# Optimization experiments

Measured on AMD Instinct MI355X. Metric: run time of the kernel, lower is better.

## Reference

```python
import jax, jax.numpy as jnp
import numpy as np
from jax.ops import segment_sum

EPS = 1e-5
N, E = 100000, 1600000
CIN, H, COUT, ED = 32, 64, 16, 16


def _lin(k, fan_in, fan_out):
    return jax.random.normal(k, (fan_in, fan_out), jnp.float32) / np.sqrt(fan_in)


def setup_inputs() -> dict:
    key = jax.random.key(0)
    ks = jax.random.split(key, 24)
    inp = {
        "x": jax.random.normal(ks[0], (N, CIN), jnp.float32),
        "edge_index": jax.random.randint(ks[1], (2, E), 0, N, jnp.int32),
        "edge_attr": jax.random.normal(ks[2], (E, ED), jnp.float32),
    }
    # layer 1 (SAGEConvWithEdgeAttr: in=CIN -> H)
    inp.update(
        l1_Wl=_lin(ks[3], CIN, H), l1_bl=jnp.zeros((H,), jnp.float32),
        l1_Wr=_lin(ks[4], CIN, H),
        l1_We=_lin(ks[5], ED, H), l1_be=jnp.zeros((H,), jnp.float32),
        l1_Wg=_lin(ks[6], 2 * H, H), l1_bg=jnp.zeros((H,), jnp.float32),
        l1_bng=jnp.ones((H,), jnp.float32), l1_bnb=jnp.zeros((H,), jnp.float32),
    )
    # layer 2 (H -> H)
    inp.update(
        l2_Wl=_lin(ks[7], H, H), l2_bl=jnp.zeros((H,), jnp.float32),
        l2_Wr=_lin(ks[8], H, H),
        l2_We=_lin(ks[9], ED, H), l2_be=jnp.zeros((H,), jnp.float32),
        l2_Wg=_lin(ks[10], 2 * H, H), l2_bg=jnp.zeros((H,), jnp.float32),
        l2_bng=jnp.ones((H,), jnp.float32), l2_bnb=jnp.zeros((H,), jnp.float32),
    )
    # GraphNorms (weight=1, bias=0, mean_scale=1 at init; randomize slightly via ones)
    inp.update(
        gn1_g=jnp.ones((H,), jnp.float32), gn1_b=jnp.zeros((H,), jnp.float32), gn1_a=jnp.ones((H,), jnp.float32),
        gn2_g=jnp.ones((H,), jnp.float32), gn2_b=jnp.zeros((H,), jnp.float32), gn2_a=jnp.ones((H,), jnp.float32),
        lin_W=_lin(ks[11], H, COUT), lin_b=jnp.zeros((COUT,), jnp.float32),
    )
    return inp


def _sage_edge_layer(x, row, col, ea, Wl, bl, Wr, We, be, Wg, bg, bng, bnb):
    n = x.shape[0]
    ea_t = ea @ We + be                                        # [E', H]
    deg = segment_sum(jnp.ones_like(col, dtype=x.dtype), col, num_segments=n)
    agg = segment_sum(x[row], col, num_segments=n) / jnp.maximum(deg, 1.0)[:, None]
    out = agg @ Wl + bl + x @ Wr                               # SAGEConv (mean)
    gate = jax.nn.sigmoid(jnp.concatenate([out[col], ea_t], -1) @ Wg + bg)
    out = out + segment_sum(gate * ea_t, col, num_segments=n)  # edge contributions
    mu = out.mean(0)
    var = ((out - mu) ** 2).mean(0)                            # BatchNorm1d (batch stats)
    out = bng * (out - mu) * jax.lax.rsqrt(var + EPS) + bnb
    return jax.nn.relu(2.0 * out)                              # Identity residual + out, relu


def _graph_norm(x, g, b, a):
    mu = x.mean(0)
    xc = x - a * mu
    var = (xc ** 2).mean(0)
    return g * xc * jax.lax.rsqrt(var + EPS) + b


def reference(x, edge_index, edge_attr,
              l1_Wl, l1_bl, l1_Wr, l1_We, l1_be, l1_Wg, l1_bg, l1_bng, l1_bnb,
              l2_Wl, l2_bl, l2_Wr, l2_We, l2_be, l2_Wg, l2_bg, l2_bng, l2_bnb,
              gn1_g, gn1_b, gn1_a, gn2_g, gn2_b, gn2_a, lin_W, lin_b):
    n = x.shape[0]
    loop = jnp.arange(n, dtype=edge_index.dtype)
    row = jnp.concatenate([edge_index[0], loop])               # add_self_loops
    col = jnp.concatenate([edge_index[1], loop])
    ea = jnp.concatenate([edge_attr, jnp.ones((n, edge_attr.shape[1]), edge_attr.dtype)], 0)
    h = _sage_edge_layer(x, row, col, ea, l1_Wl, l1_bl, l1_Wr, l1_We, l1_be, l1_Wg, l1_bg, l1_bng, l1_bnb)
    h = jax.nn.relu(h)
    h = jax.nn.relu(_graph_norm(h, gn1_g, gn1_b, gn1_a))
    h = _sage_edge_layer(h, row, col, ea, l2_Wl, l2_bl, l2_Wr, l2_We, l2_be, l2_Wg, l2_bg, l2_bng, l2_bnb)
    h = jax.nn.relu(h)
    h = jax.nn.relu(_graph_norm(h, gn2_g, gn2_b, gn2_a))
    return h @ lin_W + lin_b
```

## Files before the change

### kernel.cpp

```cpp
#include <hip/hip_runtime.h>
#include <hip/hip_fp16.h>
#include <math.h>
#include <stdint.h>

#define H 64
#define ED 16
#define CO 16
#define WGRID 2048
#define NWAVES (WGRID * 4)
#define CPART 2048
static constexpr float EPSV = 1e-5f;
static constexpr float LOG2E = 1.44269504f;

typedef _Float16 h2v __attribute__((ext_vector_type(2)));

__device__ __forceinline__ float sigm2(float z) {
    return __builtin_amdgcn_rcpf(1.0f + __builtin_amdgcn_exp2f(-z));
}

__device__ __forceinline__ h2v as_h2(int x) { union { int i; h2v h; } u; u.i = x; return u.h; }

__device__ __forceinline__ int pack2(float a, float b) {
    __half2 h = __floats2half2_rn(a, b);
    return *reinterpret_cast<int*>(&h);
}

__global__ void k_prep(const float* __restrict__ We1, const float* __restrict__ be1, const float* __restrict__ Wg1,
                       const float* __restrict__ We2, const float* __restrict__ be2, const float* __restrict__ Wg2,
                       float* __restrict__ ws) {
    int j = threadIdx.x;
    for (int l = 0; l < 2; ++l) {
        const float* We = l ? We2 : We1;
        const float* be = l ? be2 : be1;
        const float* Wg = l ? Wg2 : Wg1;
        int* wth = (int*)(ws + (l ? 1024 : 0));
        int* wgh = (int*)(ws + (l ? 1536 : 512));
        float* ets = ws + 2048 + l * 192;
        float* vs  = ws + 2112 + l * 192;
        float* dv  = ws + 2176 + l * 192;
        float wt[ED], wg[ED];
        float et = be[j];
        for (int k = 0; k < ED; ++k) { wt[k] = We[k * H + j]; et += wt[k]; }
        ets[j] = et;
        float d = 0.f;
        for (int m = 0; m < H; ++m) d += be[m] * Wg[(H + m) * H + j];
        float vsum = d;
        for (int k = 0; k < ED; ++k) {
            float acc = 0.f;
            for (int m = 0; m < H; ++m) acc += We[k * H + m] * Wg[(H + m) * H + j];
            wg[k] = acc;
            vsum += acc;
        }
        dv[j] = d * LOG2E;
        vs[j] = vsum * LOG2E;
        for (int q = 0; q < 8; ++q) {
            wth[j * 8 + q] = pack2(wt[2 * q], wt[2 * q + 1]);
            wgh[j * 8 + q] = pack2(wg[2 * q] * LOG2E, wg[2 * q + 1] * LOG2E);
        }
    }
    for (int s = 0; s < 8; ++s) ws[2432 + s * 64 + j] = 0.f;
}

__global__ void k_xh(const float* __restrict__ x, __half* __restrict__ xh, int total4) {
    int i = blockIdx.x * blockDim.x + threadIdx.x;
    if (i >= total4) return;
    float4 v = *reinterpret_cast<const float4*>(x + (size_t)i * 4);
    __half2 h0 = __floats2half2_rn(v.x, v.y), h1 = __floats2half2_rn(v.z, v.w);
    uint2 o;
    o.x = *reinterpret_cast<unsigned*>(&h0);
    o.y = *reinterpret_cast<unsigned*>(&h1);
    *reinterpret_cast<uint2*>(xh + (size_t)i * 4) = o;
}

__global__ void k_count(const int* __restrict__ cols, int* __restrict__ cnt, int E) {
    int e = blockIdx.x * blockDim.x + threadIdx.x;
    if (e < E) atomicAdd(&cnt[cols[e]], 1);
}

__global__ __launch_bounds__(1024) void k_scan1(const int* __restrict__ cnt, int* __restrict__ bs, int N) {
    __shared__ int ls[1024];
    int t = threadIdx.x;
    int i = blockIdx.x * 1024 + t;
    ls[t] = (i < N) ? cnt[i] : 0;
    __syncthreads();
    for (int off = 512; off > 0; off >>= 1) {
        if (t < off) ls[t] += ls[t + off];
        __syncthreads();
    }
    if (t == 0) bs[blockIdx.x] = ls[0];
}

__global__ __launch_bounds__(1024) void k_scan2(int* __restrict__ bs, int SB) {
    __shared__ int ls[1024];
    int t = threadIdx.x;
    int v = (t < SB) ? bs[t] : 0;
    ls[t] = v;
    __syncthreads();
    for (int off = 1; off < 1024; off <<= 1) {
        int x = (t >= off) ? ls[t - off] : 0;
        __syncthreads();
        ls[t] += x;
        __syncthreads();
    }
    if (t < SB) bs[t] = ls[t] - v;
}

__global__ __launch_bounds__(1024) void k_scan3(const int* __restrict__ cnt, const int* __restrict__ bs,
                                                int* __restrict__ rowptr, int N, int E) {
    __shared__ int ls[1024];
    int t = threadIdx.x;
    int i = blockIdx.x * 1024 + t;
    int v = (i < N) ? cnt[i] : 0;
    ls[t] = v;
    __syncthreads();
    for (int off = 1; off < 1024; off <<= 1) {
        int x = (t >= off) ? ls[t - off] : 0;
        __syncthreads();
        ls[t] += x;
        __syncthreads();
    }
    if (i < N) rowptr[i] = bs[blockIdx.x] + ls[t] - v;
    if (i == 0) rowptr[N] = E;
}

__global__ void k_ranges(const int* __restrict__ rowptr, int* __restrict__ ranges, int N, int E, int nw) {
    int w = blockIdx.x * blockDim.x + threadIdx.x;
    if (w > nw) return;
    if (w == nw) { ranges[nw] = N; return; }
    int t0 = (int)((long)E * w / nw);
    int lo = 0, hi = N;
    while (lo < hi) { int mid = (lo + hi) >> 1; if (rowptr[mid] < t0) lo = mid + 1; else hi = mid; }
    ranges[w] = lo;
}

__global__ __launch_bounds__(256) void k_part(const int* __restrict__ rows, const int* __restrict__ cols,
                                              int2* __restrict__ tmp, int* __restrict__ offtab,
                                              int E, int NB, int SH) {
    __shared__ int hist[1025];
    __shared__ int pscan[256];
    __shared__ int2 stage[CPART];
    int tid = threadIdx.x;
    int base = blockIdx.x * CPART;
    int cnt = min(CPART, E - base);
    for (int i = tid; i <= NB; i += 256) hist[i] = 0;
    __syncthreads();
    int myc[8], myr[8];
#pragma unroll
    for (int q = 0; q < 8; ++q) {
        int li = q * 256 + tid;
        if (li < cnt) {
            int e = base + li;
            myc[q] = cols[e];
            myr[q] = rows[e];
            atomicAdd(&hist[myc[q] >> SH], 1);
        } else myc[q] = -1;
    }
    __syncthreads();
    int h[4], s = 0;
    int b0 = tid * 4;
#pragma unroll
    for (int k = 0; k < 4; ++k) { h[k] = (b0 + k < NB) ? hist[b0 + k] : 0; s += h[k]; }
    pscan[tid] = s;
    __syncthreads();
    for (int off = 1; off < 256; off <<= 1) {
        int v = (tid >= off) ? pscan[tid - off] : 0;
        __syncthreads();
        pscan[tid] += v;
        __syncthreads();
    }
    int excl = pscan[tid] - s;
    __syncthreads();
    int run = excl;
#pragma unroll
    for (int k = 0; k < 4; ++k) {
        if (b0 + k < NB) hist[b0 + k] = run;
        run += h[k];
    }
    __syncthreads();
    int* ot = offtab + (size_t)blockIdx.x * (NB + 1);
    for (int i = tid; i < NB; i += 256) ot[i] = hist[i];
    if (tid == 0) ot[NB] = cnt;
    __syncthreads();
    int mask = (1 << SH) - 1;
#pragma unroll
    for (int q = 0; q < 8; ++q) {
        if (myc[q] >= 0) {
            int b = myc[q] >> SH;
            int p = atomicAdd(&hist[b], 1);
            int e = base + q * 256 + tid;
            stage[p] = make_int2(myr[q], (e << SH) | (myc[q] & mask));
        }
    }
    __syncthreads();
    int2* dst = tmp + base;
    for (int i = tid; i < cnt; i += 256) dst[i] = stage[i];
}

__global__ __launch_bounds__(256) void k_build(const int* __restrict__ rowptr, const int2* __restrict__ tmp,
                                               const int* __restrict__ offtab, const float* __restrict__ ea,
                                               int* __restrict__ erow, __half* __restrict__ eap,
                                               int N, int NB, int SH, int PB) {
    __shared__ int lcur[1024];
    int tid = threadIdx.x;
    int b = blockIdx.x;
    int NPB = 1 << SH;
    int nodelo = b << SH;
    for (int j = tid; j < NPB; j += 256) {
        int n = nodelo + j;
        lcur[j] = (n < N) ? rowptr[n] : 0;
    }
    __syncthreads();
    int mask = NPB - 1;
    for (int i = tid; i < PB; i += 256) {
        const int* ot = offtab + (size_t)i * (NB + 1);
        int j0 = ot[b], j1 = ot[b + 1];
        for (int j = j0; j < j1; ++j) {
            int2 v = tmp[(size_t)i * CPART + j];
            int e = (int)(((unsigned)v.y) >> SH);
            int cl = v.y & mask;
            int p = atomicAdd(&lcur[cl], 1);
            erow[p] = v.x;
            const float4* src = reinterpret_cast<const float4*>(ea + (size_t)e * ED);
            float4 v0 = src[0], v1 = src[1], v2 = src[2], v3 = src[3];
            int hh[8];
            hh[0] = pack2(v0.x, v0.y); hh[1] = pack2(v0.z, v0.w);
            hh[2] = pack2(v1.x, v1.y); hh[3] = pack2(v1.z, v1.w);
            hh[4] = pack2(v2.x, v2.y); hh[5] = pack2(v2.z, v2.w);
            hh[6] = pack2(v3.x, v3.y); hh[7] = pack2(v3.z, v3.w);
            const int4* o = reinterpret_cast<const int4*>(hh);
            int4* d = reinterpret_cast<int4*>(eap + (size_t)p * ED);
            d[0] = o[0]; d[1] = o[1];
        }
    }
}

template <int CIN, bool GN>
__global__ __launch_bounds__(256) void k_gather(const __half* __restrict__ x, const int* __restrict__ rowptr,
                         const int* __restrict__ ranges,
                         const int* __restrict__ erow, float* __restrict__ agg,
                         const float* __restrict__ s1, const float* __restrict__ s2,
                         const float* __restrict__ gng, const float* __restrict__ gnb,
                         const float* __restrict__ gna, float Ninv, int N) {
    int lane = threadIdx.x & 63;
    int w = (blockIdx.x * blockDim.x + threadIdx.x) >> 6;
    float A = 1.f, B = 0.f;
    if (GN) {
        float mu = s1[lane] * Ninv, m2 = s2[lane] * Ninv, a = gna[lane];
        float var = m2 - 2.f * a * mu * mu + a * a * mu * mu;
        A = gng[lane] * rsqrtf(var + EPSV);
        B = gnb[lane] - A * a * mu;
    }
    int n0 = ranges[w], n1 = ranges[w + 1];
    for (int n = n0; n < n1; ++n) {
        int s = rowptr[n], te = rowptr[n + 1];
        if (CIN == 64) {
            float raw = __half2float(x[(size_t)n * 64 + lane]);
            float acc = GN ? fmaxf(fmaf(A, raw, B), 0.f) : raw;
            int i = s;
            for (; i + 7 < te; i += 8) {
                int r0 = erow[i],     r1 = erow[i + 1], r2 = erow[i + 2], r3 = erow[i + 3];
                int r4 = erow[i + 4], r5 = erow[i + 5], r6 = erow[i + 6], r7 = erow[i + 7];
                float x0 = __half2float(x[(size_t)r0 * 64 + lane]);
                float x1 = __half2float(x[(size_t)r1 * 64 + lane]);
                float x2 = __half2float(x[(size_t)r2 * 64 + lane]);
                float x3 = __half2float(x[(size_t)r3 * 64 + lane]);
                float x4 = __half2float(x[(size_t)r4 * 64 + lane]);
                float x5 = __half2float(x[(size_t)r5 * 64 + lane]);
                float x6 = __half2float(x[(size_t)r6 * 64 + lane]);
                float x7 = __half2float(x[(size_t)r7 * 64 + lane]);
                if (GN) {
                    x0 = fmaxf(fmaf(A, x0, B), 0.f); x1 = fmaxf(fmaf(A, x1, B), 0.f);
                    x2 = fmaxf(fmaf(A, x2, B), 0.f); x3 = fmaxf(fmaf(A, x3, B), 0.f);
                    x4 = fmaxf(fmaf(A, x4, B), 0.f); x5 = fmaxf(fmaf(A, x5, B), 0.f);
                    x6 = fmaxf(fmaf(A, x6, B), 0.f); x7 = fmaxf(fmaf(A, x7, B), 0.f);
                }
                acc += ((x0 + x1) + (x2 + x3)) + ((x4 + x5) + (x6 + x7));
            }
            for (; i < te; ++i) {
                float xv = __half2float(x[(size_t)erow[i] * 64 + lane]);
                if (GN) xv = fmaxf(fmaf(A, xv, B), 0.f);
                acc += xv;
            }
            agg[(size_t)n * H + lane] = acc;
        } else {
            int c = lane & 31, half = lane >> 5;
            float acc = half ? 0.f : __half2float(x[(size_t)n * 32 + c]);
            int i = s + half;
            for (; i + 6 < te; i += 8) {
                int r0 = erow[i], r1 = erow[i + 2], r2 = erow[i + 4], r3 = erow[i + 6];
                float x0 = __half2float(x[(size_t)r0 * 32 + c]);
                float x1 = __half2float(x[(size_t)r1 * 32 + c]);
                float x2 = __half2float(x[(size_t)r2 * 32 + c]);
                float x3 = __half2float(x[(size_t)r3 * 32 + c]);
                acc += (x0 + x1) + (x2 + x3);
            }
            for (; i < te; i += 2) acc += __half2float(x[(size_t)erow[i] * 32 + c]);
            acc += __shfl_xor(acc, 32);
            if (half == 0) agg[(size_t)n * H + c] = acc;
        }
    }
}

#define MT4A(mq, aval) \
    acc[mq][0] = fmaf(aval, w1.x, acc[mq][0]); acc[mq][1] = fmaf(aval, w1.y, acc[mq][1]); \
    acc[mq][2] = fmaf(aval, w1.z, acc[mq][2]); acc[mq][3] = fmaf(aval, w1.w, acc[mq][3]);
#define MT4X(mq, aval) \
    acc[mq][0] = fmaf(aval, w2.x, acc[mq][0]); acc[mq][1] = fmaf(aval, w2.y, acc[mq][1]); \
    acc[mq][2] = fmaf(aval, w2.z, acc[mq][2]); acc[mq][3] = fmaf(aval, w2.w, acc[mq][3]);

template <int K, bool GN>
__global__ __launch_bounds__(256) void k_gemmfu(
        const float* __restrict__ A,
        const __half* __restrict__ A2, int lda2,
        const float* __restrict__ W1, const float* __restrict__ W2,
        const float* __restrict__ bias,
        const float* __restrict__ Wg, const float* __restrict__ bg,
        const float* __restrict__ s1, const float* __restrict__ s2,
        const float* __restrict__ gng, const float* __restrict__ gnb,
        const float* __restrict__ gna, float Ninv,
        const int* __restrict__ rowptr,
        __half* __restrict__ pre, __half* __restrict__ uout, int N) {
    __shared__ float WA[64 * 64];
    __shared__ float WB[K * 64];
    __shared__ float big[64][68];
    __shared__ float As[64], Bs[64], invd[64];
    int tid = threadIdx.x;
    for (int idx = tid; idx < K * 64; idx += 256) { WA[idx] = W1[idx]; WB[idx] = W2[idx]; }
    int nb = blockIdx.x * 64;
    if (tid < 64) {
        if (GN) {
            float mu = s1[tid] * Ninv, m2 = s2[tid] * Ninv, a = gna[tid];
            float var = m2 - 2.f * a * mu * mu + a * a * mu * mu;
            float Av = gng[tid] * rsqrtf(var + EPSV);
            As[tid] = Av; Bs[tid] = gnb[tid] - Av * a * mu;
        }
        int n = nb + tid;
        invd[tid] = (n < N) ? 1.f / (float)(rowptr[n + 1] - rowptr[n] + 1) : 0.f;
    }
    __syncthreads();
    int tm = tid >> 4, tn = tid & 15;
    int m0 = tm * 4, j0 = tn * 4;
    float acc[4][4];
#pragma unroll
    for (int jq = 0; jq < 4; ++jq) {
        float b = bias[j0 + jq];
#pragma unroll
        for (int mq = 0; mq < 4; ++mq) acc[mq][jq] = b;
    }
    int sn = tid >> 2, kq4 = (tid & 3) * 4;
    int sg = nb + sn;
    for (int k0 = 0; k0 < K; k0 += 16) {
        if (k0) __syncthreads();
        if (sg < N) {
            float4 av = *reinterpret_cast<const float4*>(A + (size_t)sg * 64 + k0 + kq4);
            float sc = invd[sn];
            av.x *= sc; av.y *= sc; av.z *= sc; av.w *= sc;
            big[kq4 + 0][sn] = av.x; big[kq4 + 1][sn] = av.y;
            big[kq4 + 2][sn] = av.z; big[kq4 + 3][sn] = av.w;
            uint2 hv = *reinterpret_cast<const uint2*>(A2 + (size_t)sg * lda2 + k0 + kq4);
            __half2 h01 = *reinterpret_cast<__half2*>(&hv.x);
            __half2 h23 = *reinterpret_cast<__half2*>(&hv.y);
            float2 f01 = __half22float2(h01), f23 = __half22float2(h23);
            float xv0 = f01.x, xv1 = f01.y, xv2 = f23.x, xv3 = f23.y;
            if (GN) {
                xv0 = fmaxf(fmaf(As[k0 + kq4 + 0], xv0, Bs[k0 + kq4 + 0]), 0.f);
                xv1 = fmaxf(fmaf(As[k0 + kq4 + 1], xv1, Bs[k0 + kq4 + 1]), 0.f);
                xv2 = fmaxf(fmaf(As[k0 + kq4 + 2], xv2, Bs[k0 + kq4 + 2]), 0.f);
                xv3 = fmaxf(fmaf(As[k0 + kq4 + 3], xv3, Bs[k0 + kq4 + 3]), 0.f);
            }
            big[16 + kq4 + 0][sn] = xv0; big[16 + kq4 + 1][sn] = xv1;
            big[16 + kq4 + 2][sn] = xv2; big[16 + kq4 + 3][sn] = xv3;
        } else {
#pragma unroll
            for (int q = 0; q < 4; ++q) { big[kq4 + q][sn] = 0.f; big[16 + kq4 + q][sn] = 0.f; }
        }
        __syncthreads();
#pragma unroll
        for (int k = 0; k < 16; ++k) {
            float4 am = *reinterpret_cast<const float4*>(&big[k][m0]);
            float4 w1 = *reinterpret_cast<const float4*>(&WA[(k0 + k) * 64 + j0]);
            MT4A(0, am.x) MT4A(1, am.y) MT4A(2, am.z) MT4A(3, am.w)
            float4 xm = *reinterpret_cast<const float4*>(&big[16 + k][m0]);
            float4 w2 = *reinterpret_cast<const float4*>(&WB[(k0 + k) * 64 + j0]);
            MT4X(0, xm.x) MT4X(1, xm.y) MT4X(2, xm.z) MT4X(3, xm.w)
        }
    }
    __syncthreads();
#pragma unroll
    for (int mq = 0; mq < 4; ++mq) {
        int n = nb + m0 + mq;
        if (n < N) {
            uint2 o;
            o.x = pack2(acc[mq][0], acc[mq][1]);
            o.y = pack2(acc[mq][2], acc[mq][3]);
            *reinterpret_cast<uint2*>(pre + (size_t)n * 64 + j0) = o;
        }
#pragma unroll
        for (int jq = 0; jq < 4; ++jq) big[j0 + jq][m0 + mq] = acc[mq][jq];
    }
    for (int idx = tid; idx < 4096; idx += 256) WA[idx] = Wg[idx] * LOG2E;
    __syncthreads();
    float acc2[4][4];
#pragma unroll
    for (int jq = 0; jq < 4; ++jq) {
        float b = bg[j0 + jq] * LOG2E;
#pragma unroll
        for (int mq = 0; mq < 4; ++mq) acc2[mq][jq] = b;
    }
#pragma unroll 8
    for (int k = 0; k < 64; ++k) {
        float4 pm = *reinterpret_cast<const float4*>(&big[k][m0]);
        float4 w1 = *reinterpret_cast<const float4*>(&WA[k * 64 + j0]);
        acc2[0][0] = fmaf(pm.x, w1.x, acc2[0][0]); acc2[0][1] = fmaf(pm.x, w1.y, acc2[0][1]);
        acc2[0][2] = fmaf(pm.x, w1.z, acc2[0][2]); acc2[0][3] = fmaf(pm.x, w1.w, acc2[0][3]);
        acc2[1][0] = fmaf(pm.y, w1.x, acc2[1][0]); acc2[1][1] = fmaf(pm.y, w1.y, acc2[1][1]);
        acc2[1][2] = fmaf(pm.y, w1.z, acc2[1][2]); acc2[1][3] = fmaf(pm.y, w1.w, acc2[1][3]);
        acc2[2][0] = fmaf(pm.z, w1.x, acc2[2][0]); acc2[2][1] = fmaf(pm.z, w1.y, acc2[2][1]);
        acc2[2][2] = fmaf(pm.z, w1.z, acc2[2][2]); acc2[2][3] = fmaf(pm.z, w1.w, acc2[2][3]);
        acc2[3][0] = fmaf(pm.w, w1.x, acc2[3][0]); acc2[3][1] = fmaf(pm.w, w1.y, acc2[3][1]);
        acc2[3][2] = fmaf(pm.w, w1.z, acc2[3][2]); acc2[3][3] = fmaf(pm.w, w1.w, acc2[3][3]);
    }
#pragma unroll
    for (int mq = 0; mq < 4; ++mq) {
        int n = nb + m0 + mq;
        if (n < N) {
            uint2 o;
            o.x = pack2(acc2[mq][0], acc2[mq][1]);
            o.y = pack2(acc2[mq][2], acc2[mq][3]);
            *reinterpret_cast<uint2*>(uout + (size_t)n * 64 + j0) = o;
        }
    }
}

__device__ __forceinline__ float edge_term(const int4& a, const int4& b,
                                           const h2v* wt, const h2v* wg,
                                           float be_l, float dv_l, float u_l) {
    int ua[8] = {a.x, a.y, a.z, a.w, b.x, b.y, b.z, b.w};
    float et = be_l, v = dv_l;
#pragma unroll
    for (int q = 0; q < 8; ++q) {
        h2v e = as_h2(ua[q]);
        et = __builtin_amdgcn_fdot2(e, wt[q], et, false);
        v  = __builtin_amdgcn_fdot2(e, wg[q], v, false);
    }
    return sigm2(u_l + v) * et;
}

__global__ __launch_bounds__(256) void k_gate(
        const int* __restrict__ rowptr, const int* __restrict__ ranges,
        const __half* __restrict__ eap,
        const int* __restrict__ wth, const int* __restrict__ wgh,
        const float* __restrict__ be, const float* __restrict__ dv,
        const float* __restrict__ ets, const float* __restrict__ vs,
        const __half* __restrict__ u, __half* __restrict__ pre,
        float* __restrict__ s1, float* __restrict__ s2, int N) {
    __shared__ __align__(16) int4 estage[4][128];
    __shared__ float ls[2][4][H];
    int lane = threadIdx.x & 63;
    int wv = threadIdx.x >> 6;
    int w = (blockIdx.x << 2) | wv;
    h2v wt[8], wg[8];
#pragma unroll
    for (int q = 0; q < 8; ++q) { wt[q] = as_h2(wth[lane * 8 + q]); wg[q] = as_h2(wgh[lane * 8 + q]); }
    float be_l = be[lane], dv_l = dv[lane], ets_l = ets[lane], vs_l = vs[lane];
    int n0 = ranges[w], n1 = ranges[w + 1];
    float s = 0.f, ss = 0.f;
    if (n0 < n1) {
        int4* dst = &estage[wv][0];
        const int4* gsrc = reinterpret_cast<const int4*>(eap);
        int e0 = rowptr[n0], e1 = rowptr[n1];
        int n = n0;
        int nend = rowptr[n0 + 1];
        size_t idx = (size_t)n * H + lane;
        float u_l = __half2float(u[idx]);
        float pv = __half2float(pre[idx]);
        float acc = sigm2(u_l + vs_l) * ets_l;
        {
            int bytes = min(64, e1 - e0) * 32;
            int4 p0, p1;
            if (lane * 16 < bytes) p0 = gsrc[(size_t)e0 * 2 + lane];
            if (1024 + lane * 16 < bytes) p1 = gsrc[(size_t)e0 * 2 + 64 + lane];
            if (lane * 16 < bytes) dst[lane] = p0;
            if (1024 + lane * 16 < bytes) dst[64 + lane] = p1;
        }
        for (int c = e0; c < e1; c += 64) {
            int cnt = min(64, e1 - c);
            int nbytes = (c + 64 < e1) ? min(64, e1 - c - 64) * 32 : 0;
            int4 p0, p1;
            if (lane * 16 < nbytes) p0 = gsrc[(size_t)(c + 64) * 2 + lane];
            if (1024 + lane * 16 < nbytes) p1 = gsrc[(size_t)(c + 64) * 2 + 64 + lane];
            for (int k = 0; k < cnt; ++k) {
                while (c + k == nend) {
                    float tval = pv + acc;
                    pre[idx] = __float2half(tval);
                    s += tval; ss += tval * tval;
                    ++n;
                    idx = (size_t)n * H + lane;
                    u_l = __half2float(u[idx]);
                    pv = __half2float(pre[idx]);
                    acc = sigm2(u_l + vs_l) * ets_l;
                    nend = rowptr[n + 1];
                }
                acc += edge_term(dst[k * 2], dst[k * 2 + 1], wt, wg, be_l, dv_l, u_l);
            }
            if (lane * 16 < nbytes) dst[lane] = p0;
            if (1024 + lane * 16 < nbytes) dst[64 + lane] = p1;
        }
        for (;;) {
            float tval = pv + acc;
            pre[idx] = __float2half(tval);
            s += tval; ss += tval * tval;
            ++n;
            if (n >= n1) break;
            idx = (size_t)n * H + lane;
            u_l = __half2float(u[idx]);
            pv = __half2float(pre[idx]);
            acc = sigm2(u_l + vs_l) * ets_l;
        }
    }
    ls[0][wv][lane] = s; ls[1][wv][lane] = ss;
    __syncthreads();
    if (threadIdx.x < H) {
        float a = ls[0][0][lane] + ls[0][1][lane] + ls[0][2][lane] + ls[0][3][lane];
        float b = ls[1][0][lane] + ls[1][1][lane] + ls[1][2][lane] + ls[1][3][lane];
        atomicAdd(&s1[lane], a);
        atomicAdd(&s2[lane], b);
    }
}

__global__ void k_apply(const __half* __restrict__ in, __half* __restrict__ outb,
                        const float* __restrict__ bng, const float* __restrict__ bnb,
                        const float* __restrict__ s1b, const float* __restrict__ s2b,
                        float* __restrict__ s1g, float* __restrict__ s2g, float Ninv, int N) {
    int j = threadIdx.x, ty = threadIdx.y;
    __shared__ float As[H], Bs[H];
    if (ty == 0) {
        float mu = s1b[j] * Ninv, var = s2b[j] * Ninv - mu * mu;
        float r = rsqrtf(var + EPSV);
        float A = 2.f * bng[j] * r;
        As[j] = A; Bs[j] = 2.f * (bnb[j] - bng[j] * r * mu);
    }
    __syncthreads();
    float A = As[j], B = Bs[j];
    float s = 0.f, ss = 0.f;
    for (int n = blockIdx.x * 4 + ty; n < N; n += gridDim.x * 4) {
        size_t idx = (size_t)n * H + j;
        float v = fmaxf(fmaf(A, __half2float(in[idx]), B), 0.f);
        outb[idx] = __float2half(v);
        s += v; ss += v * v;
    }
    __shared__ float ls[2][4][H];
    ls[0][ty][j] = s; ls[1][ty][j] = ss;
    __syncthreads();
    if (ty == 0) {
        float a = ls[0][0][j] + ls[0][1][j] + ls[0][2][j] + ls[0][3][j];
        float b = ls[1][0][j] + ls[1][1][j] + ls[1][2][j] + ls[1][3][j];
        atomicAdd(&s1g[j], a);
        atomicAdd(&s2g[j], b);
    }
}

__global__ __launch_bounds__(256) void k_final(const __half* __restrict__ hraw, const float* __restrict__ W,
                        const float* __restrict__ bias,
                        const float* __restrict__ s1, const float* __restrict__ s2,
                        const float* __restrict__ gng, const float* __restrict__ gnb,
                        const float* __restrict__ gna, float Ninv,
                        float* __restrict__ outp, int N) {
    __shared__ float As[H], Bs[H];
    if (threadIdx.x < H) {
        int j = threadIdx.x;
        float mu = s1[j] * Ninv, m2 = s2[j] * Ninv, a = gna[j];
        float var = m2 - 2.f * a * mu * mu + a * a * mu * mu;
        float A = gng[j] * rsqrtf(var + EPSV);
        As[j] = A; Bs[j] = gnb[j] - A * a * mu;
    }
    __syncthreads();
    int n = blockIdx.x * blockDim.x + threadIdx.x;
    if (n >= N) return;
    float o[CO];
#pragma unroll
    for (int t = 0; t < CO; ++t) o[t] = bias[t];
    const __half* hr = hraw + (size_t)n * H;
    for (int m4 = 0; m4 < H / 4; ++m4) {
        uint2 hv = *reinterpret_cast<const uint2*>(hr + m4 * 4);
        __half2 h01 = *reinterpret_cast<__half2*>(&hv.x);
        __half2 h23 = *reinterpret_cast<__half2*>(&hv.y);
        float2 f01 = __half22float2(h01), f23 = __half22float2(h23);
        float hx = fmaxf(fmaf(As[m4*4+0], f01.x, Bs[m4*4+0]), 0.f);
        float hy = fmaxf(fmaf(As[m4*4+1], f01.y, Bs[m4*4+1]), 0.f);
        float hz = fmaxf(fmaf(As[m4*4+2], f23.x, Bs[m4*4+2]), 0.f);
        float hw = fmaxf(fmaf(As[m4*4+3], f23.y, Bs[m4*4+3]), 0.f);
#pragma unroll
        for (int t = 0; t < CO; ++t) {
            o[t] += hx * W[(m4*4+0) * CO + t];
            o[t] += hy * W[(m4*4+1) * CO + t];
            o[t] += hz * W[(m4*4+2) * CO + t];
            o[t] += hw * W[(m4*4+3) * CO + t];
        }
    }
    float* orow = outp + (size_t)n * CO;
#pragma unroll
    for (int t4 = 0; t4 < CO / 4; ++t4)
        reinterpret_cast<float4*>(orow)[t4] = make_float4(o[t4*4+0], o[t4*4+1], o[t4*4+2], o[t4*4+3]);
}

extern "C" void kernel_launch(void* const* d_in, const int* in_sizes, int n_in,
                              void* d_out, int out_size, void* d_ws, size_t ws_size,
                              hipStream_t stream) {
    const float* x     = (const float*)d_in[0];
    const int*   ei    = (const int*)d_in[1];
    const float* ea    = (const float*)d_in[2];
    const float* l1_Wl = (const float*)d_in[3];  const float* l1_bl = (const float*)d_in[4];
    const float* l1_Wr = (const float*)d_in[5];  const float* l1_We = (const float*)d_in[6];
    const float* l1_be = (const float*)d_in[7];  const float* l1_Wg = (const float*)d_in[8];
    const float* l1_bg = (const float*)d_in[9];  const float* l1_bng= (const float*)d_in[10];
    const float* l1_bnb= (const float*)d_in[11];
    const float* l2_Wl = (const float*)d_in[12]; const float* l2_bl = (const float*)d_in[13];
    const float* l2_Wr = (const float*)d_in[14]; const float* l2_We = (const float*)d_in[15];
    const float* l2_be = (const float*)d_in[16]; const float* l2_Wg = (const float*)d_in[17];
    const float* l2_bg = (const float*)d_in[18]; const float* l2_bng= (const float*)d_in[19];
    const float* l2_bnb= (const float*)d_in[20];
    const float* gn1_g = (const float*)d_in[21]; const float* gn1_b = (const float*)d_in[22];
    const float* gn1_a = (const float*)d_in[23];
    const float* gn2_g = (const float*)d_in[24]; const float* gn2_b = (const float*)d_in[25];
    const float* gn2_a = (const float*)d_in[26];
    const float* lin_W = (const float*)d_in[27]; const float* lin_b = (const float*)d_in[28];

    const int N = in_sizes[0] / 32;
    const int E = in_sizes[1] / 2;
    const int* rows = ei;
    const int* cols = ei + E;

    int SH = 7, NPB = 128;
    while (((N + NPB - 1) >> SH) > 1024) { SH++; NPB <<= 1; }
    const int NB = (N + NPB - 1) >> SH;
    const int PB = (E + CPART - 1) / CPART;

    float* w    = (float*)d_ws;
    int* wth1   = (int*)w;
    int* wgh1   = (int*)(w + 512);
    int* wth2   = (int*)(w + 1024);
    int* wgh2   = (int*)(w + 1536);
    float* ets1 = w + 2048; float* vs1 = w + 2112; float* dv1 = w + 2176;
    float* ets2 = w + 2240; float* vs2 = w + 2304; float* dv2 = w + 2368;
    float* stats= w + 2432;

    int* ip     = (int*)(w + 8192);
    int* rowptr = ip;
    int* cnt    = ip + (N + 1);
    int* bs     = cnt + N;
    int* ranges = bs + 1024;
    int* erow   = ranges + (NWAVES + 2);

    uintptr_t pt = (uintptr_t)(erow + E);
    pt = (pt + 255) & ~(uintptr_t)255;
    int2* tmp = (int2*)pt;
    int* offtab = (int*)(tmp + E);
    uintptr_t pa = (uintptr_t)(offtab + (size_t)PB * (NB + 1));
    pa = (pa + 255) & ~(uintptr_t)255;
    __half* eap = (__half*)pa;
    uintptr_t pb = (uintptr_t)(eap + (size_t)E * ED);
    pb = (pb + 255) & ~(uintptr_t)255;
    float* B0 = (float*)pb;
    size_t NB64 = (size_t)N * H;
    __half* Bpre = (__half*)(B0 + NB64);
    __half* Bu   = Bpre + NB64;
    __half* xh   = Bu + NB64;
    __half* B3h  = xh + (size_t)N * 32;
    __half* B0h  = (__half*)B0;

    const float Ninv = 1.0f / (float)N;
    dim3 rb(64, 4);
    int egrid = (E + 255) / 256;
    int ngrid = (N + 255) / 256;
    int g64 = (N + 63) / 64;
    const int SB = (N + 1023) >> 10;

    k_prep<<<1, 64, 0, stream>>>(l1_We, l1_be, l1_Wg, l2_We, l2_be, l2_Wg, w);
    k_xh<<<(N * 8 + 255) / 256, 256, 0, stream>>>(x, xh, N * 8);

    hipMemsetAsync(cnt, 0, sizeof(int) * (size_t)N, stream);
    k_count<<<egrid, 256, 0, stream>>>(cols, cnt, E);
    k_scan1<<<SB, 1024, 0, stream>>>(cnt, bs, N);
    k_scan2<<<1, 1024, 0, stream>>>(bs, SB);
    k_scan3<<<SB, 1024, 0, stream>>>(cnt, bs, rowptr, N, E);
    k_ranges<<<(NWAVES + 256) / 256, 256, 0, stream>>>(rowptr, ranges, N, E, NWAVES);
    k_part<<<PB, 256, 0, stream>>>(rows, cols, tmp, offtab, E, NB, SH);
    k_build<<<NB, 256, 0, stream>>>(rowptr, tmp, offtab, ea, erow, eap, N, NB, SH, PB);

    k_gather<32, false><<<WGRID, 256, 0, stream>>>(xh, rowptr, ranges, erow, B0,
                                                   nullptr, nullptr, nullptr, nullptr, nullptr, 0.f, N);
    k_gemmfu<32, false><<<g64, 256, 0, stream>>>(B0, xh, 32, l1_Wl, l1_Wr, l1_bl, l1_Wg, l1_bg,
                                                 nullptr, nullptr, nullptr, nullptr, nullptr, 0.f,
                                                 rowptr, Bpre, Bu, N);
    k_gate<<<WGRID, 256, 0, stream>>>(rowptr, ranges, eap, wth1, wgh1, l1_be, dv1, ets1, vs1,
                                      Bu, Bpre, stats + 0, stats + 64, N);
    k_apply<<<256, rb, 0, stream>>>(Bpre, B3h, l1_bng, l1_bnb, stats + 0, stats + 64,
                                    stats + 128, stats + 192, Ninv, N);

    k_gather<64, true><<<WGRID, 256, 0, stream>>>(B3h, rowptr, ranges, erow, B0,
                                                  stats + 128, stats + 192, gn1_g, gn1_b, gn1_a, Ninv, N);
    k_gemmfu<64, true><<<g64, 256, 0, stream>>>(B0, B3h, 64, l2_Wl, l2_Wr, l2_bl, l2_Wg, l2_bg,
                                                stats + 128, stats + 192, gn1_g, gn1_b, gn1_a, Ninv,
                                                rowptr, Bpre, Bu, N);
    k_gate<<<WGRID, 256, 0, stream>>>(rowptr, ranges, eap, wth2, wgh2, l2_be, dv2, ets2, vs2,
                                      Bu, Bpre, stats + 256, stats + 320, N);
    k_apply<<<256, rb, 0, stream>>>(Bpre, B0h, l2_bng, l2_bnb, stats + 256, stats + 320,
                                    stats + 384, stats + 448, Ninv, N);

    k_final<<<ngrid, 256, 0, stream>>>(B0h, lin_W, lin_b, stats + 384, stats + 448,
                                       gn2_g, gn2_b, gn2_a, Ninv, (float*)d_out, N);
}
```

Measured before the change: 719.1 us.

## Pre-convert edge attrs to fp16, prefetch next node, unroll gate loop

Adds a separate kernel that converts edge attributes to fp16 in edge order, so the scatter in k_build moves 32 bytes per edge instead of gathering 64 bytes of fp32 at random. In k_gate, the u and pre values for the next node are now loaded ahead of time, and the inner edge loop is unrolled by two within each node's segment. The workspace layout is reshuffled so tmp, offtab and eah alias the B0 region. This costs an extra streaming pass over the edge attributes and adds aliasing risk.

```diff
diff --git a/kernel.cpp b/kernel.cpp
--- a/kernel.cpp
+++ b/kernel.cpp
@@ -72,6 +72,21 @@
     *reinterpret_cast<uint2*>(xh + (size_t)i * 4) = o;
 }
 
+__global__ void k_eah(const float* __restrict__ ea, int4* __restrict__ eah, int E) {
+    int e = blockIdx.x * blockDim.x + threadIdx.x;
+    if (e >= E) return;
+    const float4* src = reinterpret_cast<const float4*>(ea + (size_t)e * ED);
+    float4 v0 = src[0], v1 = src[1], v2 = src[2], v3 = src[3];
+    int hh[8];
+    hh[0] = pack2(v0.x, v0.y); hh[1] = pack2(v0.z, v0.w);
+    hh[2] = pack2(v1.x, v1.y); hh[3] = pack2(v1.z, v1.w);
+    hh[4] = pack2(v2.x, v2.y); hh[5] = pack2(v2.z, v2.w);
+    hh[6] = pack2(v3.x, v3.y); hh[7] = pack2(v3.z, v3.w);
+    const int4* o = reinterpret_cast<const int4*>(hh);
+    eah[(size_t)e * 2 + 0] = o[0];
+    eah[(size_t)e * 2 + 1] = o[1];
+}
+
 __global__ void k_count(const int* __restrict__ cols, int* __restrict__ cnt, int E) {
     int e = blockIdx.x * blockDim.x + threadIdx.x;
     if (e < E) atomicAdd(&cnt[cols[e]], 1);
@@ -197,7 +212,7 @@
 }
 
 __global__ __launch_bounds__(256) void k_build(const int* __restrict__ rowptr, const int2* __restrict__ tmp,
-                                               const int* __restrict__ offtab, const float* __restrict__ ea,
+                                               const int* __restrict__ offtab, const int4* __restrict__ eah,
                                                int* __restrict__ erow, __half* __restrict__ eap,
                                                int N, int NB, int SH, int PB) {
     __shared__ int lcur[1024];
@@ -220,16 +235,10 @@
             int cl = v.y & mask;
             int p = atomicAdd(&lcur[cl], 1);
             erow[p] = v.x;
-            const float4* src = reinterpret_cast<const float4*>(ea + (size_t)e * ED);
-            float4 v0 = src[0], v1 = src[1], v2 = src[2], v3 = src[3];
-            int hh[8];
-            hh[0] = pack2(v0.x, v0.y); hh[1] = pack2(v0.z, v0.w);
-            hh[2] = pack2(v1.x, v1.y); hh[3] = pack2(v1.z, v1.w);
-            hh[4] = pack2(v2.x, v2.y); hh[5] = pack2(v2.z, v2.w);
-            hh[6] = pack2(v3.x, v3.y); hh[7] = pack2(v3.z, v3.w);
-            const int4* o = reinterpret_cast<const int4*>(hh);
+            int4 a0 = eah[(size_t)e * 2 + 0];
+            int4 a1 = eah[(size_t)e * 2 + 1];
             int4* d = reinterpret_cast<int4*>(eap + (size_t)p * ED);
-            d[0] = o[0]; d[1] = o[1];
+            d[0] = a0; d[1] = a1;
         }
     }
 }
@@ -435,14 +444,23 @@
 __device__ __forceinline__ float edge_term(const int4& a, const int4& b,
                                            const h2v* wt, const h2v* wg,
                                            float be_l, float dv_l, float u_l) {
-    int ua[8] = {a.x, a.y, a.z, a.w, b.x, b.y, b.z, b.w};
     float et = be_l, v = dv_l;
-#pragma unroll
-    for (int q = 0; q < 8; ++q) {
-        h2v e = as_h2(ua[q]);
-        et = __builtin_amdgcn_fdot2(e, wt[q], et, false);
-        v  = __builtin_amdgcn_fdot2(e, wg[q], v, false);
-    }
+    et = __builtin_amdgcn_fdot2(as_h2(a.x), wt[0], et, false);
+    v  = __builtin_amdgcn_fdot2(as_h2(a.x), wg[0], v,  false);
+    et = __builtin_amdgcn_fdot2(as_h2(a.y), wt[1], et, false);
+    v  = __builtin_amdgcn_fdot2(as_h2(a.y), wg[1], v,  false);
+    et = __builtin_amdgcn_fdot2(as_h2(a.z), wt[2], et, false);
+    v  = __builtin_amdgcn_fdot2(as_h2(a.z), wg[2], v,  false);
+    et = __builtin_amdgcn_fdot2(as_h2(a.w), wt[3], et, false);
+    v  = __builtin_amdgcn_fdot2(as_h2(a.w), wg[3], v,  false);
+    et = __builtin_amdgcn_fdot2(as_h2(b.x), wt[4], et, false);
+    v  = __builtin_amdgcn_fdot2(as_h2(b.x), wg[4], v,  false);
+    et = __builtin_amdgcn_fdot2(as_h2(b.y), wt[5], et, false);
+    v  = __builtin_amdgcn_fdot2(as_h2(b.y), wg[5], v,  false);
+    et = __builtin_amdgcn_fdot2(as_h2(b.z), wt[6], et, false);
+    v  = __builtin_amdgcn_fdot2(as_h2(b.z), wg[6], v,  false);
+    et = __builtin_amdgcn_fdot2(as_h2(b.w), wt[7], et, false);
+    v  = __builtin_amdgcn_fdot2(as_h2(b.w), wg[7], v,  false);
     return sigm2(u_l + v) * et;
 }
 
@@ -474,6 +492,10 @@
         size_t idx = (size_t)n * H + lane;
         float u_l = __half2float(u[idx]);
         float pv = __half2float(pre[idx]);
+        int np = min(n + 1, n1 - 1);
+        size_t idxn = (size_t)np * H + lane;
+        float u_n = __half2float(u[idxn]);
+        float pv_n = __half2float(pre[idxn]);
         float acc = sigm2(u_l + vs_l) * ets_l;
         {
             int bytes = min(64, e1 - e0) * 32;
@@ -489,19 +511,33 @@
             int4 p0, p1;
             if (lane * 16 < nbytes) p0 = gsrc[(size_t)(c + 64) * 2 + lane];
             if (1024 + lane * 16 < nbytes) p1 = gsrc[(size_t)(c + 64) * 2 + 64 + lane];
-            for (int k = 0; k < cnt; ++k) {
+            int k = 0;
+            while (k < cnt) {
                 while (c + k == nend) {
                     float tval = pv + acc;
                     pre[idx] = __float2half(tval);
                     s += tval; ss += tval * tval;
                     ++n;
-                    idx = (size_t)n * H + lane;
-                    u_l = __half2float(u[idx]);
-                    pv = __half2float(pre[idx]);
+                    idx = idxn; u_l = u_n; pv = pv_n;
+                    np = min(n + 1, n1 - 1);
+                    idxn = (size_t)np * H + lane;
+                    u_n = __half2float(u[idxn]);
+                    pv_n = __half2float(pre[idxn]);
                     acc = sigm2(u_l + vs_l) * ets_l;
                     nend = rowptr[n + 1];
                 }
-                acc += edge_term(dst[k * 2], dst[k * 2 + 1], wt, wg, be_l, dv_l, u_l);
+                int safe = min(cnt, nend - c);
+                for (; k + 1 < safe; k += 2) {
+                    int4 d0 = dst[k * 2], d1 = dst[k * 2 + 1];
+                    int4 d2 = dst[k * 2 + 2], d3 = dst[k * 2 + 3];
+                    acc += edge_term(d0, d1, wt, wg, be_l, dv_l, u_l);
+                    acc += edge_term(d2, d3, wt, wg, be_l, dv_l, u_l);
+                }
+                if (k < safe) {
+                    int4 d0 = dst[k * 2], d1 = dst[k * 2 + 1];
+                    acc += edge_term(d0, d1, wt, wg, be_l, dv_l, u_l);
+                    ++k;
+                }
             }
             if (lane * 16 < nbytes) dst[lane] = p0;
             if (1024 + lane * 16 < nbytes) dst[64 + lane] = p1;
@@ -512,9 +548,11 @@
             s += tval; ss += tval * tval;
             ++n;
             if (n >= n1) break;
-            idx = (size_t)n * H + lane;
-            u_l = __half2float(u[idx]);
-            pv = __half2float(pre[idx]);
+            idx = idxn; u_l = u_n; pv = pv_n;
+            np = min(n + 1, n1 - 1);
+            idxn = (size_t)np * H + lane;
+            u_n = __half2float(u[idxn]);
+            pv_n = __half2float(pre[idxn]);
             acc = sigm2(u_l + vs_l) * ets_l;
         }
     }
@@ -652,21 +690,26 @@
     int* ranges = bs + 1024;
     int* erow   = ranges + (NWAVES + 2);
 
-    uintptr_t pt = (uintptr_t)(erow + E);
-    pt = (pt + 255) & ~(uintptr_t)255;
-    int2* tmp = (int2*)pt;
-    int* offtab = (int*)(tmp + E);
-    uintptr_t pa = (uintptr_t)(offtab + (size_t)PB * (NB + 1));
+    uintptr_t pa = (uintptr_t)(erow + E);
     pa = (pa + 255) & ~(uintptr_t)255;
     __half* eap = (__half*)pa;
-    uintptr_t pb = (uintptr_t)(eap + (size_t)E * ED);
-    pb = (pb + 255) & ~(uintptr_t)255;
-    float* B0 = (float*)pb;
+    uintptr_t px = (uintptr_t)(eap + (size_t)E * ED);
+    px = (px + 255) & ~(uintptr_t)255;
+    __half* xh = (__half*)px;
+    uintptr_t pz = (uintptr_t)(xh + (size_t)N * 32);
+    pz = (pz + 255) & ~(uintptr_t)255;
+
+    int2* tmp   = (int2*)pz;
+    int* offtab = (int*)(tmp + E);
+    uintptr_t pe = (uintptr_t)(offtab + (size_t)PB * (NB + 1));
+    pe = (pe + 255) & ~(uintptr_t)255;
+    int4* eah = (int4*)pe;
+
     size_t NB64 = (size_t)N * H;
+    float* B0 = (float*)pz;
     __half* Bpre = (__half*)(B0 + NB64);
     __half* Bu   = Bpre + NB64;
-    __half* xh   = Bu + NB64;
-    __half* B3h  = xh + (size_t)N * 32;
+    __half* B3h  = Bu + NB64;
     __half* B0h  = (__half*)B0;
 
     const float Ninv = 1.0f / (float)N;
@@ -678,6 +721,7 @@
 
     k_prep<<<1, 64, 0, stream>>>(l1_We, l1_be, l1_Wg, l2_We, l2_be, l2_Wg, w);
     k_xh<<<(N * 8 + 255) / 256, 256, 0, stream>>>(x, xh, N * 8);
+    k_eah<<<egrid, 256, 0, stream>>>(ea, eah, E);
 
     hipMemsetAsync(cnt, 0, sizeof(int) * (size_t)N, stream);
     k_count<<<egrid, 256, 0, stream>>>(cols, cnt, E);
@@ -686,7 +730,7 @@
     k_scan3<<<SB, 1024, 0, stream>>>(cnt, bs, rowptr, N, E);
     k_ranges<<<(NWAVES + 256) / 256, 256, 0, stream>>>(rowptr, ranges, N, E, NWAVES);
     k_part<<<PB, 256, 0, stream>>>(rows, cols, tmp, offtab, E, NB, SH);
-    k_build<<<NB, 256, 0, stream>>>(rowptr, tmp, offtab, ea, erow, eap, N, NB, SH, PB);
+    k_build<<<NB, 256, 0, stream>>>(rowptr, tmp, offtab, eah, erow, eap, N, NB, SH, PB);
 
     k_gather<32, false><<<WGRID, 256, 0, stream>>>(xh, rowptr, ranges, erow, B0,
                                                    nullptr, nullptr, nullptr, nullptr, nullptr, 0.f, N);
```

Result: no change. 713.0 us (-0.9%).
